# Kernel tuning notes

Hardware: AMD Instinct MI355X
Metric: run time of the kernel (lower is better)

Reference implementation:

```python
import jax, jax.numpy as jnp
import numpy as np

B, H, W, DIM = 16, 64, 64, 256
WS = 8
SHIFT = WS // 2
HEADS = 8
HD = DIM // HEADS
N = WS * WS            # tokens per window
MLP_H = 4 * DIM
SCALE = HD ** -0.5
NW = (H // WS) * (W // WS)


def _rel_pos_index():
    # exactly mirrors the torch buffer construction (meshgrid 'ij')
    c = np.arange(WS)
    coords = np.stack(np.meshgrid(c, c, indexing='ij'))        # (2, ws, ws)
    cf = coords.reshape(2, -1)                                 # (2, N)
    rel = (cf[:, :, None] - cf[:, None, :]).transpose(1, 2, 0).astype(np.int64)
    rel[:, :, 0] += WS - 1
    rel[:, :, 1] += WS - 1
    rel[:, :, 0] *= 2 * WS - 1
    return jnp.asarray(rel.sum(-1))                            # (N, N) int


def _attn_mask():
    # cyclic-shift mask for the shifted (SW-MSA) block
    img = np.zeros((H, W))
    sl = (slice(0, -WS), slice(-WS, -SHIFT), slice(-SHIFT, None))
    cnt = 0
    for hs in sl:
        for ws_ in sl:
            img[hs, ws_] = cnt
            cnt += 1
    mw = img.reshape(H // WS, WS, W // WS, WS).transpose(0, 2, 1, 3).reshape(-1, N)
    diff = mw[:, None, :] - mw[:, :, None]                     # (nW, N, N)
    return jnp.asarray(np.where(diff != 0, -100.0, 0.0).astype(np.float32))


REL_IDX = _rel_pos_index()
ATTN_MASK = _attn_mask()


def _ln(x, g, b):
    mu = x.mean(-1, keepdims=True)
    var = ((x - mu) ** 2).mean(-1, keepdims=True)
    return (x - mu) / jnp.sqrt(var + 1e-5) * g + b


def _block(x, p, shift, mask):
    shortcut = x                                               # (B, L, C)
    h = _ln(x, p['n1g'], p['n1b']).reshape(B, H, W, DIM)
    if shift:
        h = jnp.roll(h, (-shift, -shift), axis=(1, 2))
    # window partition -> (B*nW, N, C)
    hw = h.reshape(B, H // WS, WS, W // WS, WS, DIM).transpose(0, 1, 3, 2, 4, 5).reshape(-1, N, DIM)
    qkv = (hw @ p['qkvw'] + p['qkvb']).reshape(-1, N, 3, HEADS, HD).transpose(2, 0, 3, 1, 4)
    q, k, v = qkv[0] * SCALE, qkv[1], qkv[2]                   # (B_, heads, N, hd)
    attn = jnp.einsum('bhnd,bhmd->bhnm', q, k)
    bias = p['rpb'][REL_IDX].transpose(2, 0, 1)                # (heads, N, N)
    attn = attn + bias[None]
    if mask is not None:
        attn = attn.reshape(B, NW, HEADS, N, N) + mask[None, :, None]
        attn = attn.reshape(-1, HEADS, N, N)
    attn = jax.nn.softmax(attn, axis=-1)
    o = jnp.einsum('bhnm,bhmd->bhnd', attn, v).transpose(0, 2, 1, 3).reshape(-1, N, DIM)
    o = o @ p['pw'] + p['pb']
    # window reverse -> (B, H, W, C)
    o = o.reshape(B, H // WS, W // WS, WS, WS, DIM).transpose(0, 1, 3, 2, 4, 5).reshape(B, H, W, DIM)
    if shift:
        o = jnp.roll(o, (shift, shift), axis=(1, 2))
    x = shortcut + o.reshape(B, H * W, DIM)
    h2 = _ln(x, p['n2g'], p['n2b'])
    h2 = jax.nn.gelu(h2 @ p['f1w'] + p['f1b'], approximate=False) @ p['f2w'] + p['f2b']
    return x + h2


PARAM_NAMES = ['n1g', 'n1b', 'qkvw', 'qkvb', 'rpb', 'pw', 'pb', 'n2g', 'n2b', 'f1w', 'f1b', 'f2w', 'f2b']


def _make_params(key, blk):
    ks = jax.random.split(jax.random.fold_in(key, blk), 8)
    return {
        'n1g': jnp.ones((DIM,), jnp.float32),
        'n1b': jnp.zeros((DIM,), jnp.float32),
        'qkvw': jax.random.normal(ks[0], (DIM, 3 * DIM), jnp.float32) * 0.02,
        'qkvb': jnp.zeros((3 * DIM,), jnp.float32),
        'rpb': jax.random.normal(ks[1], ((2 * WS - 1) * (2 * WS - 1), HEADS), jnp.float32) * 0.02,
        'pw': jax.random.normal(ks[2], (DIM, DIM), jnp.float32) * 0.02,
        'pb': jnp.zeros((DIM,), jnp.float32),
        'n2g': jnp.ones((DIM,), jnp.float32),
        'n2b': jnp.zeros((DIM,), jnp.float32),
        'f1w': jax.random.normal(ks[3], (DIM, MLP_H), jnp.float32) * 0.02,
        'f1b': jnp.zeros((MLP_H,), jnp.float32),
        'f2w': jax.random.normal(ks[4], (MLP_H, DIM), jnp.float32) * 0.02,
        'f2b': jnp.zeros((DIM,), jnp.float32),
    }


def setup_inputs() -> dict:
    key = jax.random.key(0)
    inp = {'x': jax.random.normal(jax.random.fold_in(key, 100), (B, H * W, DIM), jnp.float32)}
    for blk in range(2):
        p = _make_params(key, blk)
        for n in PARAM_NAMES:
            inp[f'b{blk}_{n}'] = p[n]
    return inp


def reference(x,
              b0_n1g, b0_n1b, b0_qkvw, b0_qkvb, b0_rpb, b0_pw, b0_pb, b0_n2g, b0_n2b, b0_f1w, b0_f1b, b0_f2w, b0_f2b,
              b1_n1g, b1_n1b, b1_qkvw, b1_qkvb, b1_rpb, b1_pw, b1_pb, b1_n2g, b1_n2b, b1_f1w, b1_f1b, b1_f2w, b1_f2b):
    p0 = dict(zip(PARAM_NAMES, [b0_n1g, b0_n1b, b0_qkvw, b0_qkvb, b0_rpb, b0_pw, b0_pb, b0_n2g, b0_n2b, b0_f1w, b0_f1b, b0_f2w, b0_f2b]))
    p1 = dict(zip(PARAM_NAMES, [b1_n1g, b1_n1b, b1_qkvw, b1_qkvb, b1_rpb, b1_pw, b1_pb, b1_n2g, b1_n2b, b1_f1w, b1_f1b, b1_f2w, b1_f2b]))
    x = _block(x, p0, 0, None)          # W-MSA block
    x = _block(x, p1, SHIFT, ATTN_MASK)  # SW-MSA block
    return x
```

## Files before the change

### kernel.cpp

```cpp
#include <hip/hip_runtime.h>
#include <stdint.h>

#define ROWS 65536
#define NWT  1024
#define SCALE 0.17677669529663687f

typedef unsigned short u16;
typedef __attribute__((ext_vector_type(8))) short bf16x8;
typedef __attribute__((ext_vector_type(4))) float f32x4;
typedef __attribute__((ext_vector_type(8))) unsigned short u16x8;
typedef __attribute__((ext_vector_type(4))) unsigned short u16x4;

__device__ __forceinline__ float bf2f(u16 u){
  union { unsigned int i; float f; } c; c.i = ((unsigned int)u) << 16; return c.f;
}
__device__ __forceinline__ u16 f2bf(float f){
  union { float f; unsigned int i; } c; c.f = f;
  unsigned int r = c.i + 0x7fffu + ((c.i >> 16) & 1u);
  return (u16)(r >> 16);
}
__device__ __forceinline__ int regid(int a){ return a < 56 ? 0 : (a < 60 ? 1 : 2); }

__global__ __launch_bounds__(256) void cvt_copy(const float* __restrict__ in, float* __restrict__ out){
  int i = (blockIdx.x * 256 + threadIdx.x) * 8;
  float4 a = *(const float4*)&in[i];
  float4 b = *(const float4*)&in[i + 4];
  *(float4*)&out[i]     = a;
  *(float4*)&out[i + 4] = b;
}

__global__ __launch_bounds__(256) void transpose_all(
    const float* s0, const float* s1, const float* s2, const float* s3,
    const float* s4, const float* s5, const float* s6, const float* s7, u16* wt)
{
  __shared__ __align__(16) u16 t[32][33];
  const float* src; int K, N; size_t doff;
  switch (blockIdx.z){
    case 0: src = s0; K = 256;  N = 768;  doff = 0;               break;
    case 1: src = s1; K = 256;  N = 256;  doff = 196608;          break;
    case 2: src = s2; K = 256;  N = 1024; doff = 262144;          break;
    case 3: src = s3; K = 1024; N = 256;  doff = 524288;          break;
    case 4: src = s4; K = 256;  N = 768;  doff = 786432 + 0;      break;
    case 5: src = s5; K = 256;  N = 256;  doff = 786432 + 196608; break;
    case 6: src = s6; K = 256;  N = 1024; doff = 786432 + 262144; break;
    default:src = s7; K = 1024; N = 256;  doff = 786432 + 524288; break;
  }
  int n0 = blockIdx.x * 32, k0 = blockIdx.y * 32;
  if (n0 >= N || k0 >= K) return;
  int tx = threadIdx.x & 31, ty = threadIdx.x >> 5;
  #pragma unroll
  for (int i = 0; i < 32; i += 8) t[ty + i][tx] = f2bf(src[(size_t)(k0 + ty + i) * N + n0 + tx]);
  __syncthreads();
  u16* dst = wt + doff;
  #pragma unroll
  for (int i = 0; i < 32; i += 8) dst[(size_t)(n0 + ty + i) * K + k0 + tx] = t[tx][ty + i];
}

__global__ __launch_bounds__(256) void ln_kernel(
    const float* __restrict__ X, const float* __restrict__ g, const float* __restrict__ bt,
    u16* __restrict__ out, int windowed, int shift)
{
  int wv = (blockIdx.x * 256 + threadIdx.x) >> 6;
  int lane = threadIdx.x & 63;
  int srow;
  if (windowed){
    int win = wv >> 6, n = wv & 63;
    int b = win >> 6, wh = (win >> 3) & 7, ww = win & 7;
    int h = (wh * 8 + (n >> 3) + shift) & 63;
    int w = (ww * 8 + (n & 7) + shift) & 63;
    srow = (b << 12) + h * 64 + w;
  } else srow = wv;
  const float* xr = X + (size_t)srow * 256;
  float4 v = *(const float4*)&xr[lane * 4];
  float s  = v.x + v.y + v.z + v.w;
  float s2 = v.x * v.x + v.y * v.y + v.z * v.z + v.w * v.w;
  #pragma unroll
  for (int m = 32; m; m >>= 1){ s += __shfl_xor(s, m); s2 += __shfl_xor(s2, m); }
  float mu = s * (1.f / 256.f);
  float var = s2 * (1.f / 256.f) - mu * mu;
  float rstd = rsqrtf(var + 1e-5f);
  float4 gu = *(const float4*)&g[lane * 4];
  float4 bu = *(const float4*)&bt[lane * 4];
  u16x4 o;
  o[0] = f2bf((v.x - mu) * rstd * gu.x + bu.x);
  o[1] = f2bf((v.y - mu) * rstd * gu.y + bu.y);
  o[2] = f2bf((v.z - mu) * rstd * gu.z + bu.z);
  o[3] = f2bf((v.w - mu) * rstd * gu.w + bu.w);
  *(u16x4*)&out[(size_t)wv * 256 + lane * 4] = o;
}

template<int EPI>
__global__ __launch_bounds__(256) void gemm_bt(
    const u16* __restrict__ A, const u16* __restrict__ Bt, const float* __restrict__ bias,
    u16* __restrict__ outb, float* __restrict__ outf, float* __restrict__ X,
    int N, int K, int shift)
{
  __shared__ __align__(16) u16 As[128 * 64];
  __shared__ __align__(16) u16 Bs[128 * 64];
  int tid = threadIdx.x;
  int lane = tid & 63, wave = tid >> 6;
  int m0 = blockIdx.y * 128, n0 = blockIdx.x * 128;
  int wm = (wave >> 1) * 64, wn = (wave & 1) * 64;
  f32x4 acc[4][4];
  #pragma unroll
  for (int i = 0; i < 4; i++)
    #pragma unroll
    for (int j = 0; j < 4; j++)
      #pragma unroll
      for (int r = 0; r < 4; r++) acc[i][j][r] = 0.f;

  int lrow = tid >> 3, lcol = (tid & 7) * 8;
  const u16* Ag = A + (size_t)(m0 + lrow) * K + lcol;
  const u16* Bg = Bt + (size_t)(n0 + lrow) * K + lcol;
  u16* Asd = &As[lrow * 64 + lcol];
  u16* Bsd = &Bs[lrow * 64 + lcol];
  int r = lane & 15, koff = (lane >> 4) * 8;

  for (int kt = 0; kt < K; kt += 64){
    u16x8 ta[4], tb[4];
    #pragma unroll
    for (int i = 0; i < 4; i++) ta[i] = *(const u16x8*)(Ag + (size_t)i * 32 * K + kt);
    #pragma unroll
    for (int i = 0; i < 4; i++) tb[i] = *(const u16x8*)(Bg + (size_t)i * 32 * K + kt);
    #pragma unroll
    for (int i = 0; i < 4; i++) *(u16x8*)(Asd + i * 32 * 64) = ta[i];
    #pragma unroll
    for (int i = 0; i < 4; i++) *(u16x8*)(Bsd + i * 32 * 64) = tb[i];
    __syncthreads();
    #pragma unroll
    for (int kk = 0; kk < 64; kk += 32){
      bf16x8 af[4], bfr[4];
      #pragma unroll
      for (int i = 0; i < 4; i++) af[i]  = *(const bf16x8*)&As[(wm + i * 16 + r) * 64 + kk + koff];
      #pragma unroll
      for (int j = 0; j < 4; j++) bfr[j] = *(const bf16x8*)&Bs[(wn + j * 16 + r) * 64 + kk + koff];
      #pragma unroll
      for (int i = 0; i < 4; i++)
        #pragma unroll
        for (int j = 0; j < 4; j++)
          acc[i][j] = __builtin_amdgcn_mfma_f32_16x16x32_bf16(af[i], bfr[j], acc[i][j], 0, 0, 0);
    }
    __syncthreads();
  }

  int cq = lane >> 4, cr = lane & 15;
  #pragma unroll
  for (int j = 0; j < 4; j++){
    int col = n0 + wn + j * 16 + cr;
    float bv = bias[col];
    #pragma unroll
    for (int i = 0; i < 4; i++){
      #pragma unroll
      for (int rr = 0; rr < 4; rr++){
        int row = m0 + wm + i * 16 + cq * 4 + rr;
        float val = acc[i][j][rr] + bv;
        if (EPI == 0){
          outb[(size_t)row * N + col] = f2bf(val);
        } else if (EPI == 2){
          float gg = 0.5f * val * (1.f + erff(val * 0.70710678118f));
          outb[(size_t)row * N + col] = f2bf(gg);
        } else if (EPI == 1){
          int win = row >> 6, n = row & 63;
          int b = win >> 6, wh = (win >> 3) & 7, ww = win & 7;
          int h = (wh * 8 + (n >> 3) + shift) & 63;
          int w = (ww * 8 + (n & 7) + shift) & 63;
          X[((size_t)(b << 12) + h * 64 + w) * 256 + col] += val;
        } else if (EPI == 3){
          X[(size_t)row * 256 + col] += val;
        } else {
          outf[(size_t)row * 256 + col] = X[(size_t)row * 256 + col] + val;
        }
      }
    }
  }
}

__global__ __launch_bounds__(512) void attn_kernel(
    const u16* __restrict__ qkv, const float* __restrict__ rpb,
    u16* __restrict__ out, int shifted)
{
  __shared__ __align__(16) u16 kv_s[64 * 256];
  __shared__ float rpb_s[225 * 8];
  int win = blockIdx.x;
  int head = threadIdx.x >> 6;
  int lane = threadIdx.x & 63;

  for (int i = threadIdx.x; i < 1800; i += 512) rpb_s[i] = rpb[i];
  const u16* base = qkv + (size_t)win * 64 * 768;
  for (int ch = threadIdx.x; ch < 2048; ch += 512){
    int m = ch >> 5, c = (ch & 31) * 8;
    *(u16x8*)&kv_s[m * 256 + c] = *(const u16x8*)&base[m * 768 + 256 + c];
  }
  float q[32];
  {
    const u16* qp = base + lane * 768 + head * 32;
    #pragma unroll
    for (int d8 = 0; d8 < 32; d8 += 8){
      u16x8 u = *(const u16x8*)&qp[d8];
      #pragma unroll
      for (int jj = 0; jj < 8; jj++) q[d8 + jj] = bf2f(u[jj]) * SCALE;
    }
  }
  __syncthreads();

  int nh = lane >> 3, nw = lane & 7;
  int wh = (win >> 3) & 7, ww = win & 7;
  int idn = 0;
  if (shifted) idn = 3 * regid(wh * 8 + nh) + regid(ww * 8 + nw);

  float s[64];
  float mx = -1e30f;
  #pragma unroll
  for (int m = 0; m < 64; m++){
    float a = 0.f;
    const u16* kp = &kv_s[m * 256 + head * 32];
    #pragma unroll
    for (int d8 = 0; d8 < 32; d8 += 8){
      u16x8 u = *(const u16x8*)&kp[d8];
      #pragma unroll
      for (int jj = 0; jj < 8; jj++) a += q[d8 + jj] * bf2f(u[jj]);
    }
    int mh = m >> 3, mw = m & 7;
    a += rpb_s[((nh - mh + 7) * 15 + (nw - mw + 7)) * 8 + head];
    if (shifted){
      int idm = 3 * regid(wh * 8 + mh) + regid(ww * 8 + mw);
      if (idm != idn) a -= 100.f;
    }
    s[m] = a;
    mx = fmaxf(mx, a);
  }
  float sum = 0.f;
  #pragma unroll
  for (int m = 0; m < 64; m++){ float e = __expf(s[m] - mx); s[m] = e; sum += e; }
  float inv = 1.f / sum;

  __syncthreads();
  for (int ch = threadIdx.x; ch < 2048; ch += 512){
    int m = ch >> 5, c = (ch & 31) * 8;
    *(u16x8*)&kv_s[m * 256 + c] = *(const u16x8*)&base[m * 768 + 512 + c];
  }
  __syncthreads();

  float o[32];
  #pragma unroll
  for (int d = 0; d < 32; d++) o[d] = 0.f;
  #pragma unroll
  for (int m = 0; m < 64; m++){
    float pm = s[m];
    const u16* vp = &kv_s[m * 256 + head * 32];
    #pragma unroll
    for (int d8 = 0; d8 < 32; d8 += 8){
      u16x8 u = *(const u16x8*)&vp[d8];
      #pragma unroll
      for (int jj = 0; jj < 8; jj++) o[d8 + jj] += pm * bf2f(u[jj]);
    }
  }
  u16* op = out + (size_t)(win * 64 + lane) * 256 + head * 32;
  #pragma unroll
  for (int d8 = 0; d8 < 32; d8 += 8){
    u16x8 u;
    #pragma unroll
    for (int jj = 0; jj < 8; jj++) u[jj] = f2bf(o[d8 + jj] * inv);
    *(u16x8*)&op[d8] = u;
  }
}

extern "C" void kernel_launch(void* const* d_in, const int* in_sizes, int n_in,
                              void* d_out, int out_size, void* d_ws, size_t ws_size,
                              hipStream_t stream)
{
  const float* x = (const float*)d_in[0];
  const float* p[2][13];
  for (int blk = 0; blk < 2; blk++)
    for (int i = 0; i < 13; i++) p[blk][i] = (const float*)d_in[1 + blk * 13 + i];

  char* ws = (char*)d_ws;
  float* X  = (float*)ws;
  u16* HW   = (u16*)(ws + ((size_t)64 << 20));
  u16* BIG  = (u16*)(ws + ((size_t)96 << 20));
  u16* WT   = (u16*)(ws + ((size_t)224 << 20));

  cvt_copy<<<ROWS * 256 / (256 * 8), 256, 0, stream>>>(x, X);
  transpose_all<<<dim3(32, 32, 8), 256, 0, stream>>>(
      p[0][2], p[0][5], p[0][9], p[0][11], p[1][2], p[1][5], p[1][9], p[1][11], WT);

  for (int blk = 0; blk < 2; blk++){
    int shift = blk ? 4 : 0;
    const u16* qkvw_t = WT + (size_t)blk * 786432;
    const u16* pw_t   = WT + (size_t)blk * 786432 + 196608;
    const u16* f1w_t  = WT + (size_t)blk * 786432 + 262144;
    const u16* f2w_t  = WT + (size_t)blk * 786432 + 524288;

    ln_kernel<<<ROWS / 4, 256, 0, stream>>>(X, p[blk][0], p[blk][1], HW, 1, shift);
    gemm_bt<0><<<dim3(6, 512), 256, 0, stream>>>(HW, qkvw_t, p[blk][3], BIG, nullptr, X, 768, 256, 0);
    attn_kernel<<<NWT, 512, 0, stream>>>(BIG, p[blk][4], HW, blk);
    gemm_bt<1><<<dim3(2, 512), 256, 0, stream>>>(HW, pw_t, p[blk][6], nullptr, nullptr, X, 256, 256, shift);
    ln_kernel<<<ROWS / 4, 256, 0, stream>>>(X, p[blk][7], p[blk][8], HW, 0, 0);
    gemm_bt<2><<<dim3(8, 512), 256, 0, stream>>>(HW, f1w_t, p[blk][10], BIG, nullptr, X, 1024, 256, 0);
    if (blk == 0)
      gemm_bt<3><<<dim3(2, 512), 256, 0, stream>>>(BIG, f2w_t, p[blk][12], nullptr, nullptr, X, 256, 1024, 0);
    else
      gemm_bt<4><<<dim3(2, 512), 256, 0, stream>>>(BIG, f2w_t, p[blk][12], nullptr, (float*)d_out, X, 256, 1024, 0);
  }
}
```

Measured before the change: 1.061 ms.

## Rewrite window attention with MFMA and load GEMM tiles directly into LDS

```diff
diff --git a/kernel.cpp b/kernel.cpp
--- a/kernel.cpp
+++ b/kernel.cpp
@@ -18,6 +18,10 @@
   union { float f; unsigned int i; } c; c.f = f;
   unsigned int r = c.i + 0x7fffu + ((c.i >> 16) & 1u);
   return (u16)(r >> 16);
+}
+__device__ __forceinline__ void async_copy16(const u16* g, u16* l){
+  __builtin_amdgcn_global_load_lds((const __attribute__((address_space(1))) unsigned int*)g,
+                                   (__attribute__((address_space(3))) unsigned int*)l, 16, 0, 0);
 }
 __device__ __forceinline__ int regid(int a){ return a < 56 ? 0 : (a < 60 ? 1 : 2); }
 
@@ -117,15 +121,10 @@
   int r = lane & 15, koff = (lane >> 4) * 8;
 
   for (int kt = 0; kt < K; kt += 64){
-    u16x8 ta[4], tb[4];
-    #pragma unroll
-    for (int i = 0; i < 4; i++) ta[i] = *(const u16x8*)(Ag + (size_t)i * 32 * K + kt);
-    #pragma unroll
-    for (int i = 0; i < 4; i++) tb[i] = *(const u16x8*)(Bg + (size_t)i * 32 * K + kt);
-    #pragma unroll
-    for (int i = 0; i < 4; i++) *(u16x8*)(Asd + i * 32 * 64) = ta[i];
-    #pragma unroll
-    for (int i = 0; i < 4; i++) *(u16x8*)(Bsd + i * 32 * 64) = tb[i];
+    #pragma unroll
+    for (int i = 0; i < 4; i++) async_copy16(Ag + (size_t)i * 32 * K + kt, Asd + i * 32 * 64);
+    #pragma unroll
+    for (int i = 0; i < 4; i++) async_copy16(Bg + (size_t)i * 32 * K + kt, Bsd + i * 32 * 64);
     __syncthreads();
     #pragma unroll
     for (int kk = 0; kk < 64; kk += 32){
@@ -175,94 +174,152 @@
   }
 }
 
-__global__ __launch_bounds__(512) void attn_kernel(
+#define KS 40
+#define VS 72
+#define PS 72
+__global__ __launch_bounds__(512, 2) void attn_mfma(
     const u16* __restrict__ qkv, const float* __restrict__ rpb,
     u16* __restrict__ out, int shifted)
 {
-  __shared__ __align__(16) u16 kv_s[64 * 256];
+  __shared__ __align__(16) u16 kv_s[8 * 64 * KS];
+  __shared__ __align__(16) u16 ps[8 * 16 * PS];
   __shared__ float rpb_s[225 * 8];
+  int tid = threadIdx.x;
   int win = blockIdx.x;
-  int head = threadIdx.x >> 6;
-  int lane = threadIdx.x & 63;
-
-  for (int i = threadIdx.x; i < 1800; i += 512) rpb_s[i] = rpb[i];
+  int wv = tid >> 6;
+  int lane = tid & 63;
+  int g = lane >> 4, c = lane & 15;
   const u16* base = qkv + (size_t)win * 64 * 768;
-  for (int ch = threadIdx.x; ch < 2048; ch += 512){
-    int m = ch >> 5, c = (ch & 31) * 8;
-    *(u16x8*)&kv_s[m * 256 + c] = *(const u16x8*)&base[m * 768 + 256 + c];
-  }
-  float q[32];
-  {
-    const u16* qp = base + lane * 768 + head * 32;
-    #pragma unroll
-    for (int d8 = 0; d8 < 32; d8 += 8){
-      u16x8 u = *(const u16x8*)&qp[d8];
-      #pragma unroll
-      for (int jj = 0; jj < 8; jj++) q[d8 + jj] = bf2f(u[jj]) * SCALE;
-    }
+
+  for (int i = tid; i < 1800; i += 512) rpb_s[i] = rpb[i];
+  for (int cc = tid; cc < 2048; cc += 512){
+    int dg = cc & 3, tok = (cc >> 2) & 63, hh = cc >> 8;
+    u16x8 u = *(const u16x8*)&base[tok * 768 + 256 + hh * 32 + dg * 8];
+    *(u16x8*)&kv_s[hh * 64 * KS + tok * KS + dg * 8] = u;
   }
   __syncthreads();
 
-  int nh = lane >> 3, nw = lane & 7;
+  int h = wv;
+  bf16x8 qa[4], kb[4];
+  #pragma unroll
+  for (int i = 0; i < 4; i++)
+    qa[i] = *(const bf16x8*)&base[(i * 16 + c) * 768 + h * 32 + g * 8];
+  #pragma unroll
+  for (int j = 0; j < 4; j++)
+    kb[j] = *(const bf16x8*)&kv_s[h * 64 * KS + (j * 16 + c) * KS + g * 8];
+  f32x4 sacc[4][4];
+  #pragma unroll
+  for (int i = 0; i < 4; i++)
+    #pragma unroll
+    for (int j = 0; j < 4; j++)
+      #pragma unroll
+      for (int r = 0; r < 4; r++) sacc[i][j][r] = 0.f;
+  #pragma unroll
+  for (int i = 0; i < 4; i++)
+    #pragma unroll
+    for (int j = 0; j < 4; j++)
+      sacc[i][j] = __builtin_amdgcn_mfma_f32_16x16x32_bf16(qa[i], kb[j], sacc[i][j], 0, 0, 0);
+
   int wh = (win >> 3) & 7, ww = win & 7;
-  int idn = 0;
-  if (shifted) idn = 3 * regid(wh * 8 + nh) + regid(ww * 8 + nw);
-
-  float s[64];
-  float mx = -1e30f;
-  #pragma unroll
-  for (int m = 0; m < 64; m++){
-    float a = 0.f;
-    const u16* kp = &kv_s[m * 256 + head * 32];
-    #pragma unroll
-    for (int d8 = 0; d8 < 32; d8 += 8){
-      u16x8 u = *(const u16x8*)&kp[d8];
-      #pragma unroll
-      for (int jj = 0; jj < 8; jj++) a += q[d8 + jj] * bf2f(u[jj]);
-    }
-    int mh = m >> 3, mw = m & 7;
-    a += rpb_s[((nh - mh + 7) * 15 + (nw - mw + 7)) * 8 + head];
-    if (shifted){
-      int idm = 3 * regid(wh * 8 + mh) + regid(ww * 8 + mw);
-      if (idm != idn) a -= 100.f;
-    }
-    s[m] = a;
-    mx = fmaxf(mx, a);
-  }
-  float sum = 0.f;
-  #pragma unroll
-  for (int m = 0; m < 64; m++){ float e = __expf(s[m] - mx); s[m] = e; sum += e; }
-  float inv = 1.f / sum;
+  int mH[4], mW[4], idm[4];
+  #pragma unroll
+  for (int j = 0; j < 4; j++){
+    int m = j * 16 + c;
+    mH[j] = m >> 3; mW[j] = m & 7;
+    idm[j] = 3 * regid(wh * 8 + mH[j]) + regid(ww * 8 + mW[j]);
+  }
+  unsigned pp[4][4][2];
+  #pragma unroll
+  for (int i = 0; i < 4; i++){
+    float ex[4][4];
+    float mx[4] = {-1e30f, -1e30f, -1e30f, -1e30f};
+    #pragma unroll
+    for (int r = 0; r < 4; r++){
+      int n = i * 16 + g * 4 + r;
+      int nh = n >> 3, nw = n & 7;
+      int idn = 3 * regid(wh * 8 + nh) + regid(ww * 8 + nw);
+      #pragma unroll
+      for (int j = 0; j < 4; j++){
+        float v = sacc[i][j][r] * SCALE
+                + rpb_s[((nh - mH[j] + 7) * 15 + (nw - mW[j] + 7)) * 8 + h];
+        if (shifted && idm[j] != idn) v -= 100.f;
+        ex[j][r] = v;
+        mx[r] = fmaxf(mx[r], v);
+      }
+    }
+    #pragma unroll
+    for (int r = 0; r < 4; r++){
+      #pragma unroll
+      for (int msk = 1; msk < 16; msk <<= 1) mx[r] = fmaxf(mx[r], __shfl_xor(mx[r], msk));
+    }
+    float sm[4] = {0.f, 0.f, 0.f, 0.f};
+    #pragma unroll
+    for (int j = 0; j < 4; j++)
+      #pragma unroll
+      for (int r = 0; r < 4; r++){ ex[j][r] = __expf(ex[j][r] - mx[r]); sm[r] += ex[j][r]; }
+    #pragma unroll
+    for (int r = 0; r < 4; r++){
+      #pragma unroll
+      for (int msk = 1; msk < 16; msk <<= 1) sm[r] += __shfl_xor(sm[r], msk);
+      sm[r] = 1.f / sm[r];
+    }
+    #pragma unroll
+    for (int j = 0; j < 4; j++){
+      pp[i][j][0] = ((unsigned)f2bf(ex[j][1] * sm[1]) << 16) | f2bf(ex[j][0] * sm[0]);
+      pp[i][j][1] = ((unsigned)f2bf(ex[j][3] * sm[3]) << 16) | f2bf(ex[j][2] * sm[2]);
+    }
+  }
 
   __syncthreads();
-  for (int ch = threadIdx.x; ch < 2048; ch += 512){
-    int m = ch >> 5, c = (ch & 31) * 8;
-    *(u16x8*)&kv_s[m * 256 + c] = *(const u16x8*)&base[m * 768 + 512 + c];
+  for (int cc = tid; cc < 2048; cc += 512){
+    int tok = cc & 63, dg = (cc >> 6) & 3, hh = cc >> 8;
+    u16x8 u = *(const u16x8*)&base[tok * 768 + 512 + hh * 32 + dg * 8];
+    #pragma unroll
+    for (int j = 0; j < 8; j++)
+      kv_s[hh * 32 * VS + (dg * 8 + j) * VS + tok] = u[j];
   }
   __syncthreads();
 
-  float o[32];
-  #pragma unroll
-  for (int d = 0; d < 32; d++) o[d] = 0.f;
-  #pragma unroll
-  for (int m = 0; m < 64; m++){
-    float pm = s[m];
-    const u16* vp = &kv_s[m * 256 + head * 32];
-    #pragma unroll
-    for (int d8 = 0; d8 < 32; d8 += 8){
-      u16x8 u = *(const u16x8*)&vp[d8];
-      #pragma unroll
-      for (int jj = 0; jj < 8; jj++) o[d8 + jj] += pm * bf2f(u[jj]);
-    }
-  }
-  u16* op = out + (size_t)(win * 64 + lane) * 256 + head * 32;
-  #pragma unroll
-  for (int d8 = 0; d8 < 32; d8 += 8){
-    u16x8 u;
-    #pragma unroll
-    for (int jj = 0; jj < 8; jj++) u[jj] = f2bf(o[d8 + jj] * inv);
-    *(u16x8*)&op[d8] = u;
-  }
+  bf16x8 vb[2][2];
+  #pragma unroll
+  for (int k4 = 0; k4 < 2; k4++)
+    #pragma unroll
+    for (int t = 0; t < 2; t++)
+      vb[k4][t] = *(const bf16x8*)&kv_s[h * 32 * VS + (t * 16 + c) * VS + k4 * 32 + g * 8];
+
+  u16* pw = &ps[wv * 16 * PS];
+  f32x4 oacc[4][2];
+  #pragma unroll
+  for (int i = 0; i < 4; i++)
+    #pragma unroll
+    for (int t = 0; t < 2; t++)
+      #pragma unroll
+      for (int r = 0; r < 4; r++) oacc[i][t][r] = 0.f;
+
+  #pragma unroll
+  for (int i = 0; i < 4; i++){
+    #pragma unroll
+    for (int j = 0; j < 4; j++)
+      #pragma unroll
+      for (int r = 0; r < 4; r++)
+        pw[(g * 4 + r) * PS + j * 16 + c] = (u16)(pp[i][j][r >> 1] >> ((r & 1) * 16));
+    bf16x8 pa0 = *(const bf16x8*)&pw[c * PS + 0  + g * 8];
+    bf16x8 pa1 = *(const bf16x8*)&pw[c * PS + 32 + g * 8];
+    #pragma unroll
+    for (int t = 0; t < 2; t++){
+      oacc[i][t] = __builtin_amdgcn_mfma_f32_16x16x32_bf16(pa0, vb[0][t], oacc[i][t], 0, 0, 0);
+      oacc[i][t] = __builtin_amdgcn_mfma_f32_16x16x32_bf16(pa1, vb[1][t], oacc[i][t], 0, 0, 0);
+    }
+  }
+
+  u16* op = out + (size_t)(win * 64) * 256 + h * 32;
+  #pragma unroll
+  for (int i = 0; i < 4; i++)
+    #pragma unroll
+    for (int t = 0; t < 2; t++)
+      #pragma unroll
+      for (int r = 0; r < 4; r++)
+        op[(size_t)(i * 16 + g * 4 + r) * 256 + t * 16 + c] = f2bf(oacc[i][t][r]);
 }
 
 extern "C" void kernel_launch(void* const* d_in, const int* in_sizes, int n_in,
@@ -293,7 +350,7 @@
 
     ln_kernel<<<ROWS / 4, 256, 0, stream>>>(X, p[blk][0], p[blk][1], HW, 1, shift);
     gemm_bt<0><<<dim3(6, 512), 256, 0, stream>>>(HW, qkvw_t, p[blk][3], BIG, nullptr, X, 768, 256, 0);
-    attn_kernel<<<NWT, 512, 0, stream>>>(BIG, p[blk][4], HW, blk);
+    attn_mfma<<<NWT, 512, 0, stream>>>(BIG, p[blk][4], HW, blk);
     gemm_bt<1><<<dim3(2, 512), 256, 0, stream>>>(HW, pw_t, p[blk][6], nullptr, nullptr, X, 256, 256, shift);
     ln_kernel<<<ROWS / 4, 256, 0, stream>>>(X, p[blk][7], p[blk][8], HW, 0, 0);
     gemm_bt<2><<<dim3(8, 512), 256, 0, stream>>>(HW, f1w_t, p[blk][10], BIG, nullptr, X, 1024, 256, 0);
```

Measured after the change: 856.5 us. 19.3% less time.
